# Kernel optimization log

Hardware: AMD Instinct MI355X
Metric: run time of the kernel (lower is better)

## Reference

```python
import jax, jax.numpy as jnp
import numpy as np

N_NODES = 100000
N_EDGES = 600000
IN_CH = 128
HID = 64
NEG_SLOPE = 0.01  # nn.LeakyReLU default


def setup_inputs() -> dict:
    key = jax.random.key(0)
    k1, k2, k3, k4, k5, k6, k7, k8 = jax.random.split(key, 8)
    s1 = 1.0 / np.sqrt(IN_CH)
    s2 = 1.0 / np.sqrt(HID)
    return {
        "z": jax.random.normal(k1, (N_NODES, IN_CH), dtype=jnp.float32),
        "edge_index": jax.random.randint(k2, (2, N_EDGES), 0, N_NODES, dtype=jnp.int64),
        "W1l": jax.random.uniform(k3, (HID, IN_CH), jnp.float32, -s1, s1),
        "b1l": jax.random.uniform(k4, (HID,), jnp.float32, -s1, s1),
        "W1r": jax.random.uniform(k5, (HID, IN_CH), jnp.float32, -s1, s1),
        "b1r": jax.random.uniform(k6, (HID,), jnp.float32, -s1, s1),
        "W2": jax.random.uniform(k7, (1, HID), jnp.float32, -s2, s2),
        "b2": jax.random.uniform(k8, (1,), jnp.float32, -s2, s2),
    }


def reference(z, edge_index, W1l, b1l, W1r, b1r, W2, b2):
    # gather src/dst node features: [E, in_ch]
    zl = z[edge_index[0]]
    zr = z[edge_index[1]]
    # dual linear + add: [E, hid]
    h = jnp.einsum('ei,hi->eh', zl, W1l) + b1l + jnp.einsum('ei,hi->eh', zr, W1r) + b1r
    h = jnp.where(h >= 0, h, NEG_SLOPE * h)  # LeakyReLU
    out = jnp.einsum('eh,oh->eo', h, W2) + b2  # [E, 1]
    return jax.nn.sigmoid(out)
```

## Files before the change

kernel.cpp:

```cpp
#include <hip/hip_runtime.h>
#include <math.h>

#define N_NODES 100000
#define N_EDGES 600000
#define IN_CH 128
#define HID 64
#define NEG_SLOPE 0.01f
#define NP_GRID 1024

typedef float4 f4;
typedef unsigned short u16;
typedef unsigned int u32;
typedef __attribute__((ext_vector_type(8))) short bf16x8;
typedef __attribute__((ext_vector_type(4))) float f32x4;

__device__ __forceinline__ float lrelu(float x) {
    return fmaxf(x, NEG_SLOPE * x);
}
__device__ __forceinline__ float uasf(u32 w) { return __uint_as_float(w); }

__device__ __forceinline__ u32 cvt_pk(float lo, float hi) {
    u32 r;
    asm("v_cvt_pk_bf16_f32 %0, %1, %2" : "=v"(r) : "v"(lo), "v"(hi));
    return r;
}

__device__ __forceinline__ int load_idx(const void* ei, int is64, int pos) {
    if (is64) return (int)((const long long*)ei)[pos];
    return ((const int*)ei)[pos];
}

__device__ __forceinline__ float edot(uint4 a, uint4 b, f4 w0, f4 w1) {
    float s;
    s  = lrelu(uasf(a.x << 16) + uasf(b.x << 16)) * w0.x;
    s += lrelu(uasf(a.x & 0xffff0000u) + uasf(b.x & 0xffff0000u)) * w0.y;
    s += lrelu(uasf(a.y << 16) + uasf(b.y << 16)) * w0.z;
    s += lrelu(uasf(a.y & 0xffff0000u) + uasf(b.y & 0xffff0000u)) * w0.w;
    s += lrelu(uasf(a.z << 16) + uasf(b.z << 16)) * w1.x;
    s += lrelu(uasf(a.z & 0xffff0000u) + uasf(b.z & 0xffff0000u)) * w1.y;
    s += lrelu(uasf(a.w << 16) + uasf(b.w << 16)) * w1.z;
    s += lrelu(uasf(a.w & 0xffff0000u) + uasf(b.w & 0xffff0000u)) * w1.w;
    return s;
}

__global__ __launch_bounds__(256) void node_proj_v2(
    const float* __restrict__ z, const float* __restrict__ W1l,
    const float* __restrict__ b1l, const float* __restrict__ W1r,
    const float* __restrict__ b1r, const u32* __restrict__ ei_words,
    int* __restrict__ flag, u16* __restrict__ pcomb) {
    __shared__ uint4 zt[64 * 16];
    __shared__ u32 red;

    const int tid = threadIdx.x;

    if (blockIdx.x == 0) {
        if (tid == 0) red = 0u;
        __syncthreads();
        u32 acc = 0u;
        #pragma unroll
        for (int i = 0; i < 8; ++i)
            acc |= ei_words[(i * 256 + tid) * 2 + 1];
        atomicOr(&red, acc);
        __syncthreads();
        if (tid == 0) *flag = (red == 0u) ? 1 : 0;
    }

    const int wave = tid >> 6, lane = tid & 63;
    const int m = lane & 15, g = lane >> 4;

    bf16x8 wf[2][4];
    #pragma unroll
    for (int c2 = 0; c2 < 2; ++c2) {
        const int R = (wave << 5) + (c2 << 4) + m;
        const float* wsrc = (R < 64) ? (W1l + R * IN_CH)
                                     : (W1r + (R - 64) * IN_CH);
        #pragma unroll
        for (int kk = 0; kk < 4; ++kk) {
            const int gran = (kk << 2) | g;
            f4 a = ((const f4*)wsrc)[gran * 2];
            f4 b = ((const f4*)wsrc)[gran * 2 + 1];
            uint4 p;
            p.x = cvt_pk(a.x, a.y); p.y = cvt_pk(a.z, a.w);
            p.z = cvt_pk(b.x, b.y); p.w = cvt_pk(b.z, b.w);
            wf[c2][kk] = *(const bf16x8*)&p;
        }
    }

    const int colbase = wave << 5;
    f4 bb[2];
    #pragma unroll
    for (int c2 = 0; c2 < 2; ++c2) {
        const int col0 = colbase + (c2 << 4) + (g << 2);
        bb[c2] = *(const f4*)((colbase < 64) ? (b1l + col0) : (b1r + col0 - 64));
    }

    const int ntiles = (N_NODES + 63) / 64;
    for (int tile = blockIdx.x; tile < ntiles; tile += NP_GRID) {
        const int base = tile * 64;
        __syncthreads();
        #pragma unroll
        for (int i = 0; i < 4; ++i) {
            int gidx = tid + i * 256;
            int row = gidx >> 4, gr = gidx & 15;
            int node = base + row;
            if (node >= N_NODES) node = N_NODES - 1;
            f4 a = ((const f4*)z)[node * 32 + gr * 2];
            f4 b = ((const f4*)z)[node * 32 + gr * 2 + 1];
            uint4 p;
            p.x = cvt_pk(a.x, a.y); p.y = cvt_pk(a.z, a.w);
            p.z = cvt_pk(b.x, b.y); p.w = cvt_pk(b.z, b.w);
            zt[(row << 4) | (gr ^ (row & 15))] = p;
        }
        __syncthreads();

        f32x4 acc[4][2];
        #pragma unroll
        for (int n4 = 0; n4 < 4; ++n4)
            #pragma unroll
            for (int c2 = 0; c2 < 2; ++c2) acc[n4][c2] = {0.f, 0.f, 0.f, 0.f};

        #pragma unroll
        for (int kk = 0; kk < 4; ++kk) {
            const int gran = (kk << 2) | g;
            bf16x8 zf[4];
            #pragma unroll
            for (int n4 = 0; n4 < 4; ++n4)
                zf[n4] = *(const bf16x8*)&zt[(((n4 << 4) | m) << 4) | (gran ^ m)];
            #pragma unroll
            for (int n4 = 0; n4 < 4; ++n4)
                #pragma unroll
                for (int c2 = 0; c2 < 2; ++c2)
                    acc[n4][c2] = __builtin_amdgcn_mfma_f32_16x16x32_bf16(
                        wf[c2][kk], zf[n4], acc[n4][c2], 0, 0, 0);
        }

        #pragma unroll
        for (int c2 = 0; c2 < 2; ++c2) {
            const int col0 = colbase + (c2 << 4) + (g << 2);
            #pragma unroll
            for (int n4 = 0; n4 < 4; ++n4) {
                int node = base + (n4 << 4) + m;
                if (node < N_NODES) {
                    uint2 v;
                    v.x = cvt_pk(acc[n4][c2][0] + bb[c2].x,
                                 acc[n4][c2][1] + bb[c2].y);
                    v.y = cvt_pk(acc[n4][c2][2] + bb[c2].z,
                                 acc[n4][c2][3] + bb[c2].w);
                    *(uint2*)(pcomb + (size_t)node * 128 + col0) = v;
                }
            }
        }
    }
}

__global__ __launch_bounds__(256) void edge_quad_kernel(
    const void* __restrict__ ei, const int* __restrict__ flag,
    const u16* __restrict__ pcomb, const float* __restrict__ W2,
    const float* __restrict__ b2, float* __restrict__ out) {
    int t = blockIdx.x * 256 + threadIdx.x;
    int q = t >> 3;
    int c = t & 7;
    if (q >= N_EDGES / 4) return;
    const int is64 = *flag;
    int s[4], d[4];
    if (is64) {
        const longlong2* p = (const longlong2*)ei;
        longlong2 p0 = p[2 * q], p1 = p[2 * q + 1];
        longlong2 q0 = p[N_EDGES / 2 + 2 * q], q1 = p[N_EDGES / 2 + 2 * q + 1];
        s[0] = (int)p0.x; s[1] = (int)p0.y; s[2] = (int)p1.x; s[3] = (int)p1.y;
        d[0] = (int)q0.x; d[1] = (int)q0.y; d[2] = (int)q1.x; d[3] = (int)q1.y;
    } else {
        int4 sp = ((const int4*)ei)[q];
        int4 dp = ((const int4*)ei)[N_EDGES / 4 + q];
        s[0] = sp.x; s[1] = sp.y; s[2] = sp.z; s[3] = sp.w;
        d[0] = dp.x; d[1] = dp.y; d[2] = dp.z; d[3] = dp.w;
    }
    const uint4* pc4 = (const uint4*)pcomb;
    uint4 a0 = pc4[s[0] * 16 + c],     a1 = pc4[s[1] * 16 + c];
    uint4 a2 = pc4[s[2] * 16 + c],     a3 = pc4[s[3] * 16 + c];
    uint4 e0 = pc4[d[0] * 16 + 8 + c], e1 = pc4[d[1] * 16 + 8 + c];
    uint4 e2 = pc4[d[2] * 16 + 8 + c], e3 = pc4[d[3] * 16 + 8 + c];
    f4 w0 = ((const f4*)W2)[c * 2];
    f4 w1 = ((const f4*)W2)[c * 2 + 1];
    float r0 = edot(a0, e0, w0, w1);
    float r1 = edot(a1, e1, w0, w1);
    float r2 = edot(a2, e2, w0, w1);
    float r3 = edot(a3, e3, w0, w1);
    #pragma unroll
    for (int off = 4; off; off >>= 1) {
        r0 += __shfl_xor(r0, off, 8);
        r1 += __shfl_xor(r1, off, 8);
        r2 += __shfl_xor(r2, off, 8);
        r3 += __shfl_xor(r3, off, 8);
    }
    if (c == 0) {
        float bbs = b2[0];
        f4 o;
        o.x = 1.f / (1.f + __expf(-(r0 + bbs)));
        o.y = 1.f / (1.f + __expf(-(r1 + bbs)));
        o.z = 1.f / (1.f + __expf(-(r2 + bbs)));
        o.w = 1.f / (1.f + __expf(-(r3 + bbs)));
        *(f4*)(out + q * 4) = o;
    }
}

__global__ void detect_idx_kernel(const u32* __restrict__ ei_words,
                                  int* __restrict__ flag) {
    __shared__ u32 red;
    if (threadIdx.x == 0) red = 0u;
    __syncthreads();
    u32 acc = 0u;
    #pragma unroll
    for (int i = 0; i < 8; ++i)
        acc |= ei_words[(i * 256 + threadIdx.x) * 2 + 1];
    atomicOr(&red, acc);
    __syncthreads();
    if (threadIdx.x == 0) *flag = (red == 0u) ? 1 : 0;
}

__global__ __launch_bounds__(256) void edge_fallback_kernel(
    const float* __restrict__ z, const void* __restrict__ ei,
    const int* __restrict__ flag, const float* __restrict__ W1l,
    const float* __restrict__ b1l, const float* __restrict__ W1r,
    const float* __restrict__ b1r, const float* __restrict__ W2,
    const float* __restrict__ b2, float* __restrict__ out) {
    __shared__ f4 Wl4[64 * 32];
    __shared__ f4 Wr4[64 * 32];
    const int tid = threadIdx.x;
    #pragma unroll
    for (int i = 0; i < 8; ++i) {
        int gg = tid + i * 256;
        int h = gg >> 5, v = gg & 31;
        int slot = (h << 5) | (v ^ (h & 7));
        Wl4[slot] = ((const f4*)W1l)[gg];
        Wr4[slot] = ((const f4*)W1r)[gg];
    }
    __syncthreads();
    const int wave = tid >> 6, lane = tid & 63;
    int e = blockIdx.x * 4 + wave;
    if (e >= N_EDGES) return;
    const int is64 = (flag != nullptr) ? *flag : 0;
    int src = load_idx(ei, is64, e);
    int dst = load_idx(ei, is64, N_EDGES + e);
    float accl = 0.f, accr = 0.f;
    #pragma unroll 4
    for (int v = 0; v < 32; ++v) {
        f4 wl = Wl4[(lane << 5) | (v ^ (lane & 7))];
        f4 wr = Wr4[(lane << 5) | (v ^ (lane & 7))];
        f4 zl = ((const f4*)z)[src * 32 + v];
        f4 zr = ((const f4*)z)[dst * 32 + v];
        accl += wl.x * zl.x + wl.y * zl.y + wl.z * zl.z + wl.w * zl.w;
        accr += wr.x * zr.x + wr.y * zr.y + wr.z * zr.z + wr.w * zr.w;
    }
    float h = lrelu(accl + b1l[lane] + accr + b1r[lane]) * W2[lane];
    #pragma unroll
    for (int off = 32; off; off >>= 1) h += __shfl_xor(h, off, 64);
    if (lane == 0) out[e] = 1.f / (1.f + __expf(-(h + b2[0])));
}

extern "C" void kernel_launch(void* const* d_in, const int* in_sizes, int n_in,
                              void* d_out, int out_size, void* d_ws,
                              size_t ws_size, hipStream_t stream) {
    const float* z   = (const float*)d_in[0];
    const void*  ei  = d_in[1];
    const float* W1l = (const float*)d_in[2];
    const float* b1l = (const float*)d_in[3];
    const float* W1r = (const float*)d_in[4];
    const float* b1r = (const float*)d_in[5];
    const float* W2  = (const float*)d_in[6];
    const float* b2  = (const float*)d_in[7];
    float* out = (float*)d_out;

    const size_t pcomb_bytes = (size_t)N_NODES * 128 * sizeof(u16);
    const size_t need = pcomb_bytes + 256;

    if (ws_size >= need) {
        u16* pcomb = (u16*)d_ws;
        int* flag = (int*)((char*)d_ws + pcomb_bytes);
        node_proj_v2<<<NP_GRID, 256, 0, stream>>>(
            z, W1l, b1l, W1r, b1r, (const u32*)ei, flag, pcomb);
        edge_quad_kernel<<<(N_EDGES / 4 * 8 + 255) / 256, 256, 0, stream>>>(
            ei, flag, pcomb, W2, b2, out);
    } else if (ws_size >= 256) {
        int* flag = (int*)d_ws;
        detect_idx_kernel<<<1, 256, 0, stream>>>((const u32*)ei, flag);
        edge_fallback_kernel<<<(N_EDGES + 3) / 4, 256, 0, stream>>>(
            z, ei, flag, W1l, b1l, W1r, b1r, W2, b2, out);
    } else {
        edge_fallback_kernel<<<(N_EDGES + 3) / 4, 256, 0, stream>>>(
            z, ei, nullptr, W1l, b1l, W1r, b1r, W2, b2, out);
    }
}
```

Before: 47.29 us.

## Fold W2 into node projections and compute edge LeakyReLU dot via fp16 dot2

Node projections are now prescaled by 0.495*W2 and stored as fp16 instead of bf16. The edge kernel then rewrites LeakyReLU(h)·w as a linear term plus an |h|·sign(w) term and evaluates both with packed fp16 fdot2, replacing per-element unpack, max and multiply. Index and z loads and the output store become nontemporal. The algebraic rewrite is exact, but fp16 storage and accumulation change precision and overflow behaviour.

```diff
diff --git a/kernel.cpp b/kernel.cpp
--- a/kernel.cpp
+++ b/kernel.cpp
@@ -5,7 +5,6 @@
 #define N_EDGES 600000
 #define IN_CH 128
 #define HID 64
-#define NEG_SLOPE 0.01f
 #define NP_GRID 1024
 
 typedef float4 f4;
@@ -13,41 +12,58 @@
 typedef unsigned int u32;
 typedef __attribute__((ext_vector_type(8))) short bf16x8;
 typedef __attribute__((ext_vector_type(4))) float f32x4;
-
-__device__ __forceinline__ float lrelu(float x) {
-    return fmaxf(x, NEG_SLOPE * x);
-}
+typedef __attribute__((ext_vector_type(4))) float fv4;
+typedef __attribute__((ext_vector_type(2))) _Float16 h2;
+typedef __attribute__((ext_vector_type(2))) long long ll2;
+typedef __attribute__((ext_vector_type(4))) int iv4;
+
 __device__ __forceinline__ float uasf(u32 w) { return __uint_as_float(w); }
 
-__device__ __forceinline__ u32 cvt_pk(float lo, float hi) {
+__device__ __forceinline__ u32 cvt_pk_bf(float lo, float hi) {
     u32 r;
     asm("v_cvt_pk_bf16_f32 %0, %1, %2" : "=v"(r) : "v"(lo), "v"(hi));
     return r;
 }
+__device__ __forceinline__ u32 pk_f16(float a, float b) {
+    auto r = __builtin_amdgcn_cvt_pkrtz(a, b);
+    u32 out;
+    __builtin_memcpy(&out, &r, 4);
+    return out;
+}
+__device__ __forceinline__ h2 as_h2(u32 x) { union { u32 u; h2 h; } v; v.u = x; return v.h; }
+__device__ __forceinline__ u32 as_u32h(h2 x) { union { u32 u; h2 h; } v; v.h = x; return v.u; }
+
+__device__ __forceinline__ u32 sg2(float a, float b) {
+    u32 sa = 0x3C00u | ((__float_as_uint(a) >> 16) & 0x8000u);
+    u32 sb = 0x3C00u | ((__float_as_uint(b) >> 16) & 0x8000u);
+    return sa | (sb << 16);
+}
 
 __device__ __forceinline__ int load_idx(const void* ei, int is64, int pos) {
     if (is64) return (int)((const long long*)ei)[pos];
     return ((const int*)ei)[pos];
 }
 
-__device__ __forceinline__ float edot(uint4 a, uint4 b, f4 w0, f4 w1) {
-    float s;
-    s  = lrelu(uasf(a.x << 16) + uasf(b.x << 16)) * w0.x;
-    s += lrelu(uasf(a.x & 0xffff0000u) + uasf(b.x & 0xffff0000u)) * w0.y;
-    s += lrelu(uasf(a.y << 16) + uasf(b.y << 16)) * w0.z;
-    s += lrelu(uasf(a.y & 0xffff0000u) + uasf(b.y & 0xffff0000u)) * w0.w;
-    s += lrelu(uasf(a.z << 16) + uasf(b.z << 16)) * w1.x;
-    s += lrelu(uasf(a.z & 0xffff0000u) + uasf(b.z & 0xffff0000u)) * w1.y;
-    s += lrelu(uasf(a.w << 16) + uasf(b.w << 16)) * w1.z;
-    s += lrelu(uasf(a.w & 0xffff0000u) + uasf(b.w & 0xffff0000u)) * w1.w;
-    return s;
+__device__ __forceinline__ void eacc(uint4 a, uint4 b, const u32* sgn,
+                                     float& rlin, float& rabs) {
+    const u32* ap = (const u32*)&a;
+    const u32* bp = (const u32*)&b;
+    #pragma unroll
+    for (int k = 0; k < 4; ++k) {
+        h2 t = as_h2(ap[k]) + as_h2(bp[k]);
+        u32 tu = as_u32h(t);
+        rabs = __builtin_amdgcn_fdot2(as_h2(tu & 0x7FFF7FFFu), as_h2(sgn[k]),
+                                      rabs, false);
+        rlin = __builtin_amdgcn_fdot2(t, as_h2(0x3C003C00u), rlin, false);
+    }
 }
 
 __global__ __launch_bounds__(256) void node_proj_v2(
     const float* __restrict__ z, const float* __restrict__ W1l,
     const float* __restrict__ b1l, const float* __restrict__ W1r,
-    const float* __restrict__ b1r, const u32* __restrict__ ei_words,
-    int* __restrict__ flag, u16* __restrict__ pcomb) {
+    const float* __restrict__ b1r, const float* __restrict__ W2,
+    const u32* __restrict__ ei_words, int* __restrict__ flag,
+    u16* __restrict__ pcomb) {
     __shared__ uint4 zt[64 * 16];
     __shared__ u32 red;
 
@@ -80,20 +96,24 @@
             f4 a = ((const f4*)wsrc)[gran * 2];
             f4 b = ((const f4*)wsrc)[gran * 2 + 1];
             uint4 p;
-            p.x = cvt_pk(a.x, a.y); p.y = cvt_pk(a.z, a.w);
-            p.z = cvt_pk(b.x, b.y); p.w = cvt_pk(b.z, b.w);
+            p.x = cvt_pk_bf(a.x, a.y); p.y = cvt_pk_bf(a.z, a.w);
+            p.z = cvt_pk_bf(b.x, b.y); p.w = cvt_pk_bf(b.z, b.w);
             wf[c2][kk] = *(const bf16x8*)&p;
         }
     }
 
     const int colbase = wave << 5;
-    f4 bb[2];
+    f4 bb[2], wq[2];
     #pragma unroll
     for (int c2 = 0; c2 < 2; ++c2) {
         const int col0 = colbase + (c2 << 4) + (g << 2);
         bb[c2] = *(const f4*)((colbase < 64) ? (b1l + col0) : (b1r + col0 - 64));
-    }
-
+        f4 wv = *(const f4*)(W2 + (col0 & 63));
+        wq[c2].x = 0.495f * wv.x; wq[c2].y = 0.495f * wv.y;
+        wq[c2].z = 0.495f * wv.z; wq[c2].w = 0.495f * wv.w;
+    }
+
+    const fv4* zp = (const fv4*)z;
     const int ntiles = (N_NODES + 63) / 64;
     for (int tile = blockIdx.x; tile < ntiles; tile += NP_GRID) {
         const int base = tile * 64;
@@ -104,11 +124,11 @@
             int row = gidx >> 4, gr = gidx & 15;
             int node = base + row;
             if (node >= N_NODES) node = N_NODES - 1;
-            f4 a = ((const f4*)z)[node * 32 + gr * 2];
-            f4 b = ((const f4*)z)[node * 32 + gr * 2 + 1];
+            fv4 a = __builtin_nontemporal_load(&zp[node * 32 + gr * 2]);
+            fv4 b = __builtin_nontemporal_load(&zp[node * 32 + gr * 2 + 1]);
             uint4 p;
-            p.x = cvt_pk(a.x, a.y); p.y = cvt_pk(a.z, a.w);
-            p.z = cvt_pk(b.x, b.y); p.w = cvt_pk(b.z, b.w);
+            p.x = cvt_pk_bf(a[0], a[1]); p.y = cvt_pk_bf(a[2], a[3]);
+            p.z = cvt_pk_bf(b[0], b[1]); p.w = cvt_pk_bf(b[2], b[3]);
             zt[(row << 4) | (gr ^ (row & 15))] = p;
         }
         __syncthreads();
@@ -142,10 +162,10 @@
                 int node = base + (n4 << 4) + m;
                 if (node < N_NODES) {
                     uint2 v;
-                    v.x = cvt_pk(acc[n4][c2][0] + bb[c2].x,
-                                 acc[n4][c2][1] + bb[c2].y);
-                    v.y = cvt_pk(acc[n4][c2][2] + bb[c2].z,
-                                 acc[n4][c2][3] + bb[c2].w);
+                    v.x = pk_f16((acc[n4][c2][0] + bb[c2].x) * wq[c2].x,
+                                 (acc[n4][c2][1] + bb[c2].y) * wq[c2].y);
+                    v.y = pk_f16((acc[n4][c2][2] + bb[c2].z) * wq[c2].z,
+                                 (acc[n4][c2][3] + bb[c2].w) * wq[c2].w);
                     *(uint2*)(pcomb + (size_t)node * 128 + col0) = v;
                 }
             }
@@ -162,30 +182,46 @@
     int c = t & 7;
     if (q >= N_EDGES / 4) return;
     const int is64 = *flag;
+
+    f4 wa = ((const f4*)W2)[c * 2];
+    f4 wb = ((const f4*)W2)[c * 2 + 1];
+    u32 sgn[4];
+    sgn[0] = sg2(wa.x, wa.y); sgn[1] = sg2(wa.z, wa.w);
+    sgn[2] = sg2(wb.x, wb.y); sgn[3] = sg2(wb.z, wb.w);
+
     int s[4], d[4];
     if (is64) {
-        const longlong2* p = (const longlong2*)ei;
-        longlong2 p0 = p[2 * q], p1 = p[2 * q + 1];
-        longlong2 q0 = p[N_EDGES / 2 + 2 * q], q1 = p[N_EDGES / 2 + 2 * q + 1];
-        s[0] = (int)p0.x; s[1] = (int)p0.y; s[2] = (int)p1.x; s[3] = (int)p1.y;
-        d[0] = (int)q0.x; d[1] = (int)q0.y; d[2] = (int)q1.x; d[3] = (int)q1.y;
+        const ll2* p = (const ll2*)ei;
+        ll2 p0 = __builtin_nontemporal_load(&p[2 * q]);
+        ll2 p1 = __builtin_nontemporal_load(&p[2 * q + 1]);
+        ll2 q0 = __builtin_nontemporal_load(&p[N_EDGES / 2 + 2 * q]);
+        ll2 q1 = __builtin_nontemporal_load(&p[N_EDGES / 2 + 2 * q + 1]);
+        s[0] = (int)p0[0]; s[1] = (int)p0[1]; s[2] = (int)p1[0]; s[3] = (int)p1[1];
+        d[0] = (int)q0[0]; d[1] = (int)q0[1]; d[2] = (int)q1[0]; d[3] = (int)q1[1];
     } else {
-        int4 sp = ((const int4*)ei)[q];
-        int4 dp = ((const int4*)ei)[N_EDGES / 4 + q];
-        s[0] = sp.x; s[1] = sp.y; s[2] = sp.z; s[3] = sp.w;
-        d[0] = dp.x; d[1] = dp.y; d[2] = dp.z; d[3] = dp.w;
+        const iv4* p = (const iv4*)ei;
+        iv4 sp = __builtin_nontemporal_load(&p[q]);
+        iv4 dp = __builtin_nontemporal_load(&p[N_EDGES / 4 + q]);
+        s[0] = sp[0]; s[1] = sp[1]; s[2] = sp[2]; s[3] = sp[3];
+        d[0] = dp[0]; d[1] = dp[1]; d[2] = dp[2]; d[3] = dp[3];
     }
     const uint4* pc4 = (const uint4*)pcomb;
     uint4 a0 = pc4[s[0] * 16 + c],     a1 = pc4[s[1] * 16 + c];
     uint4 a2 = pc4[s[2] * 16 + c],     a3 = pc4[s[3] * 16 + c];
     uint4 e0 = pc4[d[0] * 16 + 8 + c], e1 = pc4[d[1] * 16 + 8 + c];
     uint4 e2 = pc4[d[2] * 16 + 8 + c], e3 = pc4[d[3] * 16 + 8 + c];
-    f4 w0 = ((const f4*)W2)[c * 2];
-    f4 w1 = ((const f4*)W2)[c * 2 + 1];
-    float r0 = edot(a0, e0, w0, w1);
-    float r1 = edot(a1, e1, w0, w1);
-    float r2 = edot(a2, e2, w0, w1);
-    float r3 = edot(a3, e3, w0, w1);
+
+    float rl0 = 0.f, ra0 = 0.f, rl1 = 0.f, ra1 = 0.f;
+    float rl2 = 0.f, ra2 = 0.f, rl3 = 0.f, ra3 = 0.f;
+    eacc(a0, e0, sgn, rl0, ra0);
+    eacc(a1, e1, sgn, rl1, ra1);
+    eacc(a2, e2, sgn, rl2, ra2);
+    eacc(a3, e3, sgn, rl3, ra3);
+    const float K = 1.02020202020202f;
+    float r0 = fmaf(rl0, K, ra0);
+    float r1 = fmaf(rl1, K, ra1);
+    float r2 = fmaf(rl2, K, ra2);
+    float r3 = fmaf(rl3, K, ra3);
     #pragma unroll
     for (int off = 4; off; off >>= 1) {
         r0 += __shfl_xor(r0, off, 8);
@@ -195,14 +231,16 @@
     }
     if (c == 0) {
         float bbs = b2[0];
-        f4 o;
-        o.x = 1.f / (1.f + __expf(-(r0 + bbs)));
-        o.y = 1.f / (1.f + __expf(-(r1 + bbs)));
-        o.z = 1.f / (1.f + __expf(-(r2 + bbs)));
-        o.w = 1.f / (1.f + __expf(-(r3 + bbs)));
-        *(f4*)(out + q * 4) = o;
-    }
-}
+        fv4 o;
+        o[0] = 1.f / (1.f + __expf(-(r0 + bbs)));
+        o[1] = 1.f / (1.f + __expf(-(r1 + bbs)));
+        o[2] = 1.f / (1.f + __expf(-(r2 + bbs)));
+        o[3] = 1.f / (1.f + __expf(-(r3 + bbs)));
+        __builtin_nontemporal_store(o, (fv4*)(out + q * 4));
+    }
+}
+
+__device__ __forceinline__ float lrelu(float x) { return fmaxf(x, 0.01f * x); }
 
 __global__ void detect_idx_kernel(const u32* __restrict__ ei_words,
                                   int* __restrict__ flag) {
@@ -278,7 +316,7 @@
         u16* pcomb = (u16*)d_ws;
         int* flag = (int*)((char*)d_ws + pcomb_bytes);
         node_proj_v2<<<NP_GRID, 256, 0, stream>>>(
-            z, W1l, b1l, W1r, b1r, (const u32*)ei, flag, pcomb);
+            z, W1l, b1l, W1r, b1r, W2, (const u32*)ei, flag, pcomb);
         edge_quad_kernel<<<(N_EDGES / 4 * 8 + 255) / 256, 256, 0, stream>>>(
             ei, flag, pcomb, W2, b2, out);
     } else if (ws_size >= 256) {
```

After: 54.87 us. +16.0%, slower.
